# Kernel tuning notes

Hardware: AMD Instinct MI355X
Metric: run time of the kernel (lower is better)

Reference implementation:

```python
import jax, jax.numpy as jnp
import numpy as np

N = 50000   # nodes
E = 800000  # edges per edge type
H = 4       # attention heads
C = 64      # per-head out channels
EPS = 1e-5  # batchnorm eps


def gat_conv(x, ei, W, a_s, a_d, b):
    # PyG GATConv with add_self_loops=True, concat=True, negative_slope=0.2
    h = (x @ W).reshape(-1, H, C)                      # [N,H,C]
    sl = jnp.arange(N)
    src = jnp.concatenate([ei[0], sl])                 # [E+N]
    dst = jnp.concatenate([ei[1], sl])
    al_s = (h * a_s).sum(-1)                           # [N,H]
    al_d = (h * a_d).sum(-1)
    e = jax.nn.leaky_relu(al_s[src] + al_d[dst], 0.2)  # [E+N,H]
    m = jax.ops.segment_max(e, dst, num_segments=N)    # segment softmax over dst
    ex = jnp.exp(e - m[dst])
    s = jax.ops.segment_sum(ex, dst, num_segments=N)
    alpha = ex / (s[dst] + 1e-16)                      # [E+N,H]
    out = jax.ops.segment_sum(alpha[:, :, None] * h[src], dst, num_segments=N)
    return out.reshape(N, H * C) + b


def bn(x, g, b):
    mu = x.mean(0)
    v = jnp.var(x, 0)
    return g * (x - mu) * jax.lax.rsqrt(v + EPS) + b


def setup_inputs() -> dict:
    key = jax.random.key(0)
    ks = jax.random.split(key, 20)
    p = {}
    p["x"] = jax.random.normal(ks[0], (N, 128), jnp.float32)
    p["edge_index_spatial"] = jax.random.randint(ks[1], (2, E), 0, N)
    p["edge_index_temporal"] = jax.random.randint(ks[2], (2, E), 0, N)
    ins = [128, 256, 256, 256]
    k = 3
    for i in range(4):
        sc = 1.0 / np.sqrt(ins[i]).astype(np.float32)
        p[f"W{i+1}"] = jax.random.normal(ks[k], (ins[i], H * C), jnp.float32) * sc; k += 1
        p[f"as{i+1}"] = jax.random.normal(ks[k], (H, C), jnp.float32) * 0.1; k += 1
        p[f"ad{i+1}"] = jax.random.normal(ks[k], (H, C), jnp.float32) * 0.1; k += 1
        p[f"b{i+1}"] = jnp.zeros((H * C,), jnp.float32)
        p[f"g{i+1}"] = jnp.ones((H * C,), jnp.float32)
        p[f"be{i+1}"] = jnp.zeros((H * C,), jnp.float32)
    p["Wl"] = jax.random.normal(ks[k], (H * C, 32), jnp.float32) * (1.0 / 16.0)
    p["bl"] = jnp.zeros((32,), jnp.float32)
    return p


def reference(x, edge_index_spatial, edge_index_temporal,
              W1, as1, ad1, b1, g1, be1,
              W2, as2, ad2, b2, g2, be2,
              W3, as3, ad3, b3, g3, be3,
              W4, as4, ad4, b4, g4, be4,
              Wl, bl):
    h = jax.nn.relu(bn(gat_conv(x, edge_index_spatial, W1, as1, ad1, b1), g1, be1))
    h = jax.nn.relu(bn(gat_conv(h, edge_index_spatial, W2, as2, ad2, b2), g2, be2))
    h = jax.nn.relu(bn(gat_conv(h, edge_index_temporal, W3, as3, ad3, b3), g3, be3))
    h = jax.nn.relu(bn(gat_conv(h, edge_index_temporal, W4, as4, ad4, b4), g4, be4))
    return h @ Wl + bl
```

## Files before the change

kernel.cpp:

```cpp
#include <hip/hip_runtime.h>
#include <hip/hip_bf16.h>
#include <hip/hip_fp16.h>
#include <math.h>

#define N_NODES 50000
#define N_EDGES 800000
#define NH 4
#define HC 256
#define TOT_E (N_EDGES + N_NODES)
#define SCAN_NB ((N_NODES + 255) / 256)

typedef __attribute__((ext_vector_type(8))) short short8;
typedef __attribute__((ext_vector_type(4))) float f32x4;

static __device__ __forceinline__ float lrelu(float x) { return x >= 0.f ? x : 0.2f * x; }

static __device__ __forceinline__ unsigned short bf16_rne(float x) {
    unsigned int u = __float_as_uint(x);
    u += 0x7fff + ((u >> 16) & 1);
    return (unsigned short)(u >> 16);
}

__global__ __launch_bounds__(256) void count_kernel(const int* __restrict__ ei,
                                                    int* __restrict__ cnt) {
    int i = blockIdx.x * blockDim.x + threadIdx.x;
    if (i >= TOT_E) return;
    int dst = (i < N_EDGES) ? ei[N_EDGES + i] : (i - N_EDGES);
    atomicAdd(&cnt[dst], 1);
}

__global__ __launch_bounds__(256) void scan1_kernel(const int* __restrict__ cnt,
                                                    int* __restrict__ offs,
                                                    int* __restrict__ bsum) {
    __shared__ int sm[256];
    const int t = threadIdx.x;
    const int base = blockIdx.x * 256;
    int v = (base + t < N_NODES) ? cnt[base + t] : 0;
    sm[t] = v;
    __syncthreads();
#pragma unroll
    for (int d = 1; d < 256; d <<= 1) {
        int add = (t >= d) ? sm[t - d] : 0;
        __syncthreads();
        sm[t] += add;
        __syncthreads();
    }
    if (base + t < N_NODES) offs[base + t] = sm[t] - v;
    if (t == 255) bsum[blockIdx.x] = sm[255];
}

__global__ __launch_bounds__(256) void scan2_kernel(int* __restrict__ bsum,
                                                    int* __restrict__ total) {
    __shared__ int sm[256];
    const int t = threadIdx.x;
    int v = (t < SCAN_NB) ? bsum[t] : 0;
    sm[t] = v;
    __syncthreads();
#pragma unroll
    for (int d = 1; d < 256; d <<= 1) {
        int add = (t >= d) ? sm[t - d] : 0;
        __syncthreads();
        sm[t] += add;
        __syncthreads();
    }
    if (t < SCAN_NB) bsum[t] = sm[t] - v;
    if (t == 255) *total = sm[255];
}

__global__ __launch_bounds__(256) void scan3_kernel(int* __restrict__ offs,
                                                    const int* __restrict__ bsum) {
    int i = blockIdx.x * blockDim.x + threadIdx.x;
    if (i < N_NODES) offs[i] += bsum[i >> 8];
}

__global__ __launch_bounds__(256) void scatter_kernel(const int* __restrict__ ei,
                                                      const int* __restrict__ offs,
                                                      int* __restrict__ cursor,
                                                      int* __restrict__ ssrc) {
    int i = blockIdx.x * blockDim.x + threadIdx.x;
    if (i >= TOT_E) return;
    int src, dst;
    if (i < N_EDGES) { src = ei[i]; dst = ei[N_EDGES + i]; }
    else             { src = i - N_EDGES; dst = src; }
    int pos = offs[dst] + atomicAdd(&cursor[dst], 1);
    ssrc[pos] = src;
}

__global__ __launch_bounds__(256) void gemm_kernel(const float* __restrict__ A,
                                                   const float* __restrict__ B,
                                                   __half* __restrict__ C,
                                                   const float* __restrict__ bnscale,
                                                   const float* __restrict__ bnshift,
                                                   const float* __restrict__ a_s,
                                                   const float* __restrict__ a_d,
                                                   float* __restrict__ als,
                                                   float* __restrict__ ald,
                                                   int M, int K) {
    __shared__ unsigned short Ah[128][40], Al[128][40];
    __shared__ unsigned short Bh[128][40], Bl[128][40];
    const int t = threadIdx.x;
    const int l = t & 63;
    const int w = t >> 6;
    const int wr = w >> 1, wc = w & 1;
    const int fr = l & 15;
    const int kg = (l >> 4) << 3;
    const int bm = blockIdx.x * 128;
    const int bn = blockIdx.y * 128;
    const int ra = t >> 1, ka = (t & 1) << 4;
    const int nb = (t & 31) << 2, kb = (t >> 5) << 2;

    f32x4 acc[4][4] = {};

    for (int k0 = 0; k0 < K; k0 += 32) {
        {
            const int row = bm + ra;
#pragma unroll
            for (int i = 0; i < 4; ++i) {
                const int kk = ka + 4 * i;
                float4 a4 = make_float4(0.f, 0.f, 0.f, 0.f);
                if (row < M) a4 = *(const float4*)(A + (size_t)row * K + k0 + kk);
                if (bnscale) {
                    float4 sc = *(const float4*)(bnscale + k0 + kk);
                    float4 sh = *(const float4*)(bnshift + k0 + kk);
                    a4.x = fmaxf(0.f, fmaf(a4.x, sc.x, sh.x));
                    a4.y = fmaxf(0.f, fmaf(a4.y, sc.y, sh.y));
                    a4.z = fmaxf(0.f, fmaf(a4.z, sc.z, sh.z));
                    a4.w = fmaxf(0.f, fmaf(a4.w, sc.w, sh.w));
                }
                unsigned short h[4], lo[4];
                float v[4] = {a4.x, a4.y, a4.z, a4.w};
#pragma unroll
                for (int q = 0; q < 4; ++q) {
                    h[q] = bf16_rne(v[q]);
                    float hf = __uint_as_float((unsigned int)h[q] << 16);
                    lo[q] = bf16_rne(v[q] - hf);
                }
                *(uint2*)&Ah[ra][kk] = *(uint2*)h;
                *(uint2*)&Al[ra][kk] = *(uint2*)lo;
            }
        }
        {
            float4 bv[4];
#pragma unroll
            for (int i = 0; i < 4; ++i)
                bv[i] = *(const float4*)(B + (size_t)(k0 + kb + i) * HC + bn + nb);
#pragma unroll
            for (int c = 0; c < 4; ++c) {
                float v[4] = {c == 0 ? bv[0].x : c == 1 ? bv[0].y : c == 2 ? bv[0].z : bv[0].w,
                              c == 0 ? bv[1].x : c == 1 ? bv[1].y : c == 2 ? bv[1].z : bv[1].w,
                              c == 0 ? bv[2].x : c == 1 ? bv[2].y : c == 2 ? bv[2].z : bv[2].w,
                              c == 0 ? bv[3].x : c == 1 ? bv[3].y : c == 2 ? bv[3].z : bv[3].w};
                unsigned short h[4], lo[4];
#pragma unroll
                for (int q = 0; q < 4; ++q) {
                    h[q] = bf16_rne(v[q]);
                    float hf = __uint_as_float((unsigned int)h[q] << 16);
                    lo[q] = bf16_rne(v[q] - hf);
                }
                *(uint2*)&Bh[nb + c][kb] = *(uint2*)h;
                *(uint2*)&Bl[nb + c][kb] = *(uint2*)lo;
            }
        }
        __syncthreads();
        short8 ahf[4], alf[4], bhf[4], blf[4];
#pragma unroll
        for (int m = 0; m < 4; ++m) {
            ahf[m] = *(const short8*)&Ah[wr * 64 + m * 16 + fr][kg];
            alf[m] = *(const short8*)&Al[wr * 64 + m * 16 + fr][kg];
        }
#pragma unroll
        for (int n = 0; n < 4; ++n) {
            bhf[n] = *(const short8*)&Bh[wc * 64 + n * 16 + fr][kg];
            blf[n] = *(const short8*)&Bl[wc * 64 + n * 16 + fr][kg];
        }
#pragma unroll
        for (int m = 0; m < 4; ++m)
#pragma unroll
            for (int n = 0; n < 4; ++n) {
                acc[m][n] = __builtin_amdgcn_mfma_f32_16x16x32_bf16(ahf[m], bhf[n], acc[m][n], 0, 0, 0);
                acc[m][n] = __builtin_amdgcn_mfma_f32_16x16x32_bf16(ahf[m], blf[n], acc[m][n], 0, 0, 0);
                acc[m][n] = __builtin_amdgcn_mfma_f32_16x16x32_bf16(alf[m], bhf[n], acc[m][n], 0, 0, 0);
            }
        __syncthreads();
    }

#pragma unroll
    for (int m = 0; m < 4; ++m) {
        const int row0 = bm + wr * 64 + m * 16 + ((l >> 4) << 2);
#pragma unroll
        for (int n = 0; n < 4; ++n) {
            const int col = bn + wc * 64 + n * 16 + fr;
#pragma unroll
            for (int r = 0; r < 4; ++r) {
                if (row0 + r < M)
                    C[(size_t)(row0 + r) * HC + col] = __float2half(acc[m][n][r]);
            }
        }
    }
    const int hw = (bn >> 6) + wc;
    float asv[4], adv[4];
#pragma unroll
    for (int n = 0; n < 4; ++n) {
        const int col = bn + wc * 64 + n * 16 + fr;
        asv[n] = a_s[col];
        adv[n] = a_d[col];
    }
#pragma unroll
    for (int m = 0; m < 4; ++m) {
        const int row0 = bm + wr * 64 + m * 16 + ((l >> 4) << 2);
#pragma unroll
        for (int r = 0; r < 4; ++r) {
            float ps = 0.f, pd = 0.f;
#pragma unroll
            for (int n = 0; n < 4; ++n) {
                ps = fmaf(acc[m][n][r], asv[n], ps);
                pd = fmaf(acc[m][n][r], adv[n], pd);
            }
#pragma unroll
            for (int d = 1; d < 16; d <<= 1) {
                ps += __shfl_xor(ps, d, 64);
                pd += __shfl_xor(pd, d, 64);
            }
            if (fr == 0 && row0 + r < M) {
                als[(row0 + r) * NH + hw] = ps;
                ald[(row0 + r) * NH + hw] = pd;
            }
        }
    }
}

__global__ __launch_bounds__(256) void gat_edge_kernel(const __half* __restrict__ h,
                                                       const int* __restrict__ offs,
                                                       const int* __restrict__ ssrc,
                                                       const float* __restrict__ als,
                                                       const float* __restrict__ ald,
                                                       const float* __restrict__ bias,
                                                       float* __restrict__ out) {
    __shared__ float ex_sm[4][64][NH];
    __shared__ int   src_sm[4][64];
    const int lane = threadIdx.x & 63;
    const int w = threadIdx.x >> 6;
    const int v = (blockIdx.x << 2) + w;
    if (v >= N_NODES) return;
    const int hh = lane >> 4;
    const float4 aldv4 = *(const float4*)(ald + v * NH);
    const int beg = offs[v], end = offs[v + 1];

    float4 m4 = make_float4(-INFINITY, -INFINITY, -INFINITY, -INFINITY);
    float4 s4 = make_float4(0.f, 0.f, 0.f, 0.f);
    float ax = 0.f, ay = 0.f, az = 0.f, aw = 0.f;

    for (int c0 = beg; c0 < end; c0 += 64) {
        const int n = min(64, end - c0);
        const int s0 = ssrc[c0];
        int srcl = s0;
        float4 e4 = make_float4(-INFINITY, -INFINITY, -INFINITY, -INFINITY);
        if (lane < n) {
            srcl = ssrc[c0 + lane];
            float4 a4 = *(const float4*)(als + srcl * NH);
            e4.x = lrelu(a4.x + aldv4.x);
            e4.y = lrelu(a4.y + aldv4.y);
            e4.z = lrelu(a4.z + aldv4.z);
            e4.w = lrelu(a4.w + aldv4.w);
        }
        float4 cm = e4;
#pragma unroll
        for (int d = 1; d < 64; d <<= 1) {
            cm.x = fmaxf(cm.x, __shfl_xor(cm.x, d, 64));
            cm.y = fmaxf(cm.y, __shfl_xor(cm.y, d, 64));
            cm.z = fmaxf(cm.z, __shfl_xor(cm.z, d, 64));
            cm.w = fmaxf(cm.w, __shfl_xor(cm.w, d, 64));
        }
        const float4 mn = make_float4(fmaxf(m4.x, cm.x), fmaxf(m4.y, cm.y),
                                      fmaxf(m4.z, cm.z), fmaxf(m4.w, cm.w));
        const float4 r4 = make_float4(__expf(m4.x - mn.x), __expf(m4.y - mn.y),
                                      __expf(m4.z - mn.z), __expf(m4.w - mn.w));
        float4 ex4;
        ex4.x = __expf(e4.x - mn.x);
        ex4.y = __expf(e4.y - mn.y);
        ex4.z = __expf(e4.z - mn.z);
        ex4.w = __expf(e4.w - mn.w);
        src_sm[w][lane] = srcl;
        *(float4*)&ex_sm[w][lane][0] = ex4;
        float4 se = ex4;
#pragma unroll
        for (int d = 1; d < 64; d <<= 1) {
            se.x += __shfl_xor(se.x, d, 64);
            se.y += __shfl_xor(se.y, d, 64);
            se.z += __shfl_xor(se.z, d, 64);
            se.w += __shfl_xor(se.w, d, 64);
        }
        s4 = make_float4(fmaf(s4.x, r4.x, se.x), fmaf(s4.y, r4.y, se.y),
                         fmaf(s4.z, r4.z, se.z), fmaf(s4.w, r4.w, se.w));
        const float rh = hh == 0 ? r4.x : hh == 1 ? r4.y : hh == 2 ? r4.z : r4.w;
        ax *= rh; ay *= rh; az *= rh; aw *= rh;
        m4 = mn;

        const int trip = (n + 7) & ~7;
        int sj[8]; float wj[8];
#pragma unroll
        for (int q = 0; q < 8; ++q) { sj[q] = src_sm[w][q]; wj[q] = ex_sm[w][q][hh]; }
        const int co = lane << 2;
        for (int j = 0; j < trip; j += 8) {
            uint2 raw[8];
#pragma unroll
            for (int q = 0; q < 8; ++q)
                raw[q] = *(const uint2*)(h + (size_t)sj[q] * HC + co);
            float u[8];
#pragma unroll
            for (int q = 0; q < 8; ++q) u[q] = wj[q];
            if (j + 8 < trip) {
#pragma unroll
                for (int q = 0; q < 8; ++q) {
                    sj[q] = src_sm[w][j + 8 + q];
                    wj[q] = ex_sm[w][j + 8 + q][hh];
                }
            }
#pragma unroll
            for (int q = 0; q < 8; ++q) {
                const __half2 lo = *reinterpret_cast<const __half2*>(&raw[q].x);
                const __half2 hi = *reinterpret_cast<const __half2*>(&raw[q].y);
                const float2 f0 = __half22float2(lo);
                const float2 f1 = __half22float2(hi);
                ax = fmaf(u[q], f0.x, ax); ay = fmaf(u[q], f0.y, ay);
                az = fmaf(u[q], f1.x, az); aw = fmaf(u[q], f1.y, aw);
            }
        }
    }

    const float sh = hh == 0 ? s4.x : hh == 1 ? s4.y : hh == 2 ? s4.z : s4.w;
    const float inv = 1.f / (sh + 1e-16f);
    const float4 b4 = *(const float4*)(bias + (lane << 2));
    *(float4*)(out + (size_t)v * HC + (lane << 2)) =
        make_float4(fmaf(ax, inv, b4.x), fmaf(ay, inv, b4.y),
                    fmaf(az, inv, b4.z), fmaf(aw, inv, b4.w));
}

__global__ __launch_bounds__(256) void bn_stats_kernel(const float* __restrict__ y,
                                                       double* __restrict__ sum,
                                                       double* __restrict__ sqsum) {
    const int t = threadIdx.x;
    const int r0 = blockIdx.x * 128;
    const int r1 = min(r0 + 128, N_NODES);
    float s = 0.f, q = 0.f;
    for (int r = r0; r < r1; ++r) {
        float v = y[(size_t)r * HC + t];
        s += v;
        q = fmaf(v, v, q);
    }
    atomicAdd(&sum[t], (double)s);
    atomicAdd(&sqsum[t], (double)q);
}

__global__ void bn_finalize_kernel(const double* __restrict__ sum,
                                   const double* __restrict__ sqsum,
                                   const float* __restrict__ g,
                                   const float* __restrict__ be,
                                   float* __restrict__ scale,
                                   float* __restrict__ shift) {
    int t = threadIdx.x;
    double mean = sum[t] / (double)N_NODES;
    double var = sqsum[t] / (double)N_NODES - mean * mean;
    float sc = g[t] * rsqrtf((float)var + 1e-5f);
    scale[t] = sc;
    shift[t] = be[t] - (float)mean * sc;
}

__global__ __launch_bounds__(256) void linear_kernel(const float* __restrict__ y,
                                                     const float* __restrict__ Wl,
                                                     const float* __restrict__ bl,
                                                     const float* __restrict__ scale,
                                                     const float* __restrict__ shift,
                                                     float* __restrict__ out) {
    __shared__ float Wls[256 * 32];
    __shared__ float scs[256], shs[256];
    const int t = threadIdx.x;
    for (int i = t; i < 256 * 32; i += 256) Wls[i] = Wl[i];
    scs[t] = scale[t];
    shs[t] = shift[t];
    __syncthreads();
    int gid = blockIdx.x * 256 + t;
    if (gid >= N_NODES * 32) return;
    int n = gid >> 5, j = gid & 31;
    float acc = bl[j];
    const float4* yrow = (const float4*)(y + (size_t)n * HC);
#pragma unroll
    for (int k4 = 0; k4 < 64; ++k4) {
        float4 y4 = yrow[k4];
        int k = k4 << 2;
        y4.x = fmaxf(0.f, fmaf(y4.x, scs[k + 0], shs[k + 0]));
        y4.y = fmaxf(0.f, fmaf(y4.y, scs[k + 1], shs[k + 1]));
        y4.z = fmaxf(0.f, fmaf(y4.z, scs[k + 2], shs[k + 2]));
        y4.w = fmaxf(0.f, fmaf(y4.w, scs[k + 3], shs[k + 3]));
        acc = fmaf(y4.x, Wls[(k + 0) * 32 + j], acc);
        acc = fmaf(y4.y, Wls[(k + 1) * 32 + j], acc);
        acc = fmaf(y4.z, Wls[(k + 2) * 32 + j], acc);
        acc = fmaf(y4.w, Wls[(k + 3) * 32 + j], acc);
    }
    out[gid] = acc;
}

extern "C" void kernel_launch(void* const* d_in, const int* in_sizes, int n_in,
                              void* d_out, int out_size, void* d_ws, size_t ws_size,
                              hipStream_t stream) {
    const float* x     = (const float*)d_in[0];
    const int* ei_sp   = (const int*)d_in[1];
    const int* ei_tp   = (const int*)d_in[2];
    const float* Wl    = (const float*)d_in[27];
    const float* bl    = (const float*)d_in[28];

    char* ws = (char*)d_ws;
    size_t off = 0;
    auto alloc = [&](size_t bytes) -> char* {
        char* p = ws + off;
        off = (off + bytes + 255) & ~(size_t)255;
        return p;
    };
    __half* buf0   = (__half*)alloc((size_t)N_NODES * HC * 2);
    float* buf1    = (float*)alloc((size_t)N_NODES * HC * 4);
    float* als     = (float*)alloc((size_t)N_NODES * NH * 4);
    float* ald     = (float*)alloc((size_t)N_NODES * NH * 4);
    int*   offs_sp = (int*)alloc((size_t)(N_NODES + 1) * 4);
    int*   offs_tp = (int*)alloc((size_t)(N_NODES + 1) * 4);
    int*   src_sp  = (int*)alloc((size_t)TOT_E * 4);
    int*   src_tp  = (int*)alloc((size_t)TOT_E * 4);
    int*   cnt     = (int*)alloc((size_t)N_NODES * 4);
    int*   bsum    = (int*)alloc((size_t)SCAN_NB * 4);
    double* bnsum  = (double*)alloc(256 * 8 * 2);
    double* bnsq   = bnsum + 256;
    float* scale   = (float*)alloc(256 * 4);
    float* shift   = (float*)alloc(256 * 4);
    (void)ws_size; (void)in_sizes; (void)n_in; (void)out_size;

    const int EB = (TOT_E + 255) / 256;

    hipMemsetAsync(cnt, 0, (size_t)N_NODES * 4, stream);
    count_kernel<<<EB, 256, 0, stream>>>(ei_sp, cnt);
    scan1_kernel<<<SCAN_NB, 256, 0, stream>>>(cnt, offs_sp, bsum);
    scan2_kernel<<<1, 256, 0, stream>>>(bsum, offs_sp + N_NODES);
    scan3_kernel<<<SCAN_NB, 256, 0, stream>>>(offs_sp, bsum);
    hipMemsetAsync(cnt, 0, (size_t)N_NODES * 4, stream);
    scatter_kernel<<<EB, 256, 0, stream>>>(ei_sp, offs_sp, cnt, src_sp);

    hipMemsetAsync(cnt, 0, (size_t)N_NODES * 4, stream);
    count_kernel<<<EB, 256, 0, stream>>>(ei_tp, cnt);
    scan1_kernel<<<SCAN_NB, 256, 0, stream>>>(cnt, offs_tp, bsum);
    scan2_kernel<<<1, 256, 0, stream>>>(bsum, offs_tp + N_NODES);
    scan3_kernel<<<SCAN_NB, 256, 0, stream>>>(offs_tp, bsum);
    hipMemsetAsync(cnt, 0, (size_t)N_NODES * 4, stream);
    scatter_kernel<<<EB, 256, 0, stream>>>(ei_tp, offs_tp, cnt, src_tp);

    const int NB4 = (N_NODES + 3) / 4;
    const dim3 ggrid((N_NODES + 127) / 128, 2);
    for (int L = 0; L < 4; ++L) {
        const float* in = (L == 0) ? x : buf1;
        const int K = (L == 0) ? 128 : 256;
        const float* bns = (L == 0) ? nullptr : scale;
        const float* bnh = (L == 0) ? nullptr : shift;
        const int* offs = (L < 2) ? offs_sp : offs_tp;
        const int* ssrc = (L < 2) ? src_sp : src_tp;
        const int base = 3 + L * 6;
        const float* W  = (const float*)d_in[base + 0];
        const float* as_ = (const float*)d_in[base + 1];
        const float* ad_ = (const float*)d_in[base + 2];
        const float* b_  = (const float*)d_in[base + 3];
        const float* g_  = (const float*)d_in[base + 4];
        const float* be_ = (const float*)d_in[base + 5];

        gemm_kernel<<<ggrid, 256, 0, stream>>>(in, W, buf0, bns, bnh,
                                               as_, ad_, als, ald, N_NODES, K);
        gat_edge_kernel<<<NB4, 256, 0, stream>>>(buf0, offs, ssrc, als, ald, b_, buf1);

        hipMemsetAsync(bnsum, 0, 256 * 8 * 2, stream);
        bn_stats_kernel<<<(N_NODES + 127) / 128, 256, 0, stream>>>(buf1, bnsum, bnsq);
        bn_finalize_kernel<<<1, 256, 0, stream>>>(bnsum, bnsq, g_, be_, scale, shift);
    }

    linear_kernel<<<(N_NODES * 32 + 255) / 256, 256, 0, stream>>>(buf1, Wl, bl,
                                                                  scale, shift,
                                                                  (float*)d_out);
}
```

Measured before the change: 1.057 ms.

## Merge CSR builds, pre-split GEMM operands to bf16 hi/lo, widen edge gather

Builds both edge-type CSR structures in a single set of count/scan/scatter launches. Splits activations and weights into bf16 hi/lo arrays in separate kernels so the GEMM only does vector loads of bf16 data. The edge aggregation kernel now gathers 16-byte rows, with two edges processed per wave half. BN finalize is folded into the split and linear kernels. This removes launches and per-tile conversion work but adds an extra pass over activations and more workspace.

```diff
diff --git a/kernel.cpp b/kernel.cpp
--- a/kernel.cpp
+++ b/kernel.cpp
@@ -8,24 +8,32 @@
 #define NH 4
 #define HC 256
 #define TOT_E (N_EDGES + N_NODES)
-#define SCAN_NB ((N_NODES + 255) / 256)
+#define NT2 (2 * N_NODES)
+#define NB2 ((NT2 + 255) / 256)
 
 typedef __attribute__((ext_vector_type(8))) short short8;
 typedef __attribute__((ext_vector_type(4))) float f32x4;
+typedef unsigned short ushort_t;
 
 static __device__ __forceinline__ float lrelu(float x) { return x >= 0.f ? x : 0.2f * x; }
 
-static __device__ __forceinline__ unsigned short bf16_rne(float x) {
+static __device__ __forceinline__ ushort_t bf16_rne(float x) {
     unsigned int u = __float_as_uint(x);
     u += 0x7fff + ((u >> 16) & 1);
-    return (unsigned short)(u >> 16);
-}
-
-__global__ __launch_bounds__(256) void count_kernel(const int* __restrict__ ei,
-                                                    int* __restrict__ cnt) {
+    return (ushort_t)(u >> 16);
+}
+
+__global__ __launch_bounds__(256) void count2_kernel(const int* __restrict__ ei_sp,
+                                                     const int* __restrict__ ei_tp,
+                                                     int* __restrict__ cnt) {
     int i = blockIdx.x * blockDim.x + threadIdx.x;
-    if (i >= TOT_E) return;
-    int dst = (i < N_EDGES) ? ei[N_EDGES + i] : (i - N_EDGES);
+    if (i >= 2 * TOT_E) return;
+    int dst;
+    if (i < TOT_E) dst = (i < N_EDGES) ? ei_sp[N_EDGES + i] : (i - N_EDGES);
+    else {
+        int j = i - TOT_E;
+        dst = N_NODES + ((j < N_EDGES) ? ei_tp[N_EDGES + j] : (j - N_EDGES));
+    }
     atomicAdd(&cnt[dst], 1);
 }
 
@@ -35,7 +43,7 @@
     __shared__ int sm[256];
     const int t = threadIdx.x;
     const int base = blockIdx.x * 256;
-    int v = (base + t < N_NODES) ? cnt[base + t] : 0;
+    int v = (base + t < NT2) ? cnt[base + t] : 0;
     sm[t] = v;
     __syncthreads();
 #pragma unroll
@@ -45,59 +53,142 @@
         sm[t] += add;
         __syncthreads();
     }
-    if (base + t < N_NODES) offs[base + t] = sm[t] - v;
+    if (base + t < NT2) offs[base + t] = sm[t] - v;
     if (t == 255) bsum[blockIdx.x] = sm[255];
 }
 
-__global__ __launch_bounds__(256) void scan2_kernel(int* __restrict__ bsum,
+__global__ __launch_bounds__(512) void scan2_kernel(int* __restrict__ bsum,
                                                     int* __restrict__ total) {
-    __shared__ int sm[256];
+    __shared__ int sm[512];
     const int t = threadIdx.x;
-    int v = (t < SCAN_NB) ? bsum[t] : 0;
+    int v = (t < NB2) ? bsum[t] : 0;
     sm[t] = v;
     __syncthreads();
 #pragma unroll
-    for (int d = 1; d < 256; d <<= 1) {
+    for (int d = 1; d < 512; d <<= 1) {
         int add = (t >= d) ? sm[t - d] : 0;
         __syncthreads();
         sm[t] += add;
         __syncthreads();
     }
-    if (t < SCAN_NB) bsum[t] = sm[t] - v;
-    if (t == 255) *total = sm[255];
+    if (t < NB2) bsum[t] = sm[t] - v;
+    if (t == 511) *total = sm[511];
 }
 
 __global__ __launch_bounds__(256) void scan3_kernel(int* __restrict__ offs,
                                                     const int* __restrict__ bsum) {
     int i = blockIdx.x * blockDim.x + threadIdx.x;
-    if (i < N_NODES) offs[i] += bsum[i >> 8];
-}
-
-__global__ __launch_bounds__(256) void scatter_kernel(const int* __restrict__ ei,
-                                                      const int* __restrict__ offs,
-                                                      int* __restrict__ cursor,
-                                                      int* __restrict__ ssrc) {
+    if (i < NT2) offs[i] += bsum[i >> 8];
+}
+
+__global__ __launch_bounds__(256) void scatter2_kernel(const int* __restrict__ ei_sp,
+                                                       const int* __restrict__ ei_tp,
+                                                       const int* __restrict__ offs,
+                                                       int* __restrict__ cursor,
+                                                       int* __restrict__ ssrc) {
     int i = blockIdx.x * blockDim.x + threadIdx.x;
-    if (i >= TOT_E) return;
-    int src, dst;
-    if (i < N_EDGES) { src = ei[i]; dst = ei[N_EDGES + i]; }
-    else             { src = i - N_EDGES; dst = src; }
-    int pos = offs[dst] + atomicAdd(&cursor[dst], 1);
+    if (i >= 2 * TOT_E) return;
+    int src, dstIdx;
+    if (i < TOT_E) {
+        src = (i < N_EDGES) ? ei_sp[i] : (i - N_EDGES);
+        dstIdx = (i < N_EDGES) ? ei_sp[N_EDGES + i] : (i - N_EDGES);
+    } else {
+        int j = i - TOT_E;
+        src = (j < N_EDGES) ? ei_tp[j] : (j - N_EDGES);
+        dstIdx = N_NODES + ((j < N_EDGES) ? ei_tp[N_EDGES + j] : (j - N_EDGES));
+    }
+    int pos = offs[dstIdx] + atomicAdd(&cursor[dstIdx], 1);
     ssrc[pos] = src;
 }
 
-__global__ __launch_bounds__(256) void gemm_kernel(const float* __restrict__ A,
-                                                   const float* __restrict__ B,
+__global__ __launch_bounds__(256) void split_x_kernel(const float* __restrict__ x,
+                                                      ushort_t* __restrict__ Ah,
+                                                      ushort_t* __restrict__ Al) {
+    int i = blockIdx.x * 256 + threadIdx.x;
+    float4 v = ((const float4*)x)[i];
+    float a[4] = {v.x, v.y, v.z, v.w};
+    ushort_t h[4], lo[4];
+#pragma unroll
+    for (int q = 0; q < 4; ++q) {
+        h[q] = bf16_rne(a[q]);
+        float hf = __uint_as_float((unsigned int)h[q] << 16);
+        lo[q] = bf16_rne(a[q] - hf);
+    }
+    *(uint2*)(Ah + (size_t)i * 4) = *(uint2*)h;
+    *(uint2*)(Al + (size_t)i * 4) = *(uint2*)lo;
+}
+
+__global__ __launch_bounds__(256) void split_h_kernel(const float* __restrict__ y,
+                                                      const double* __restrict__ sum,
+                                                      const double* __restrict__ sqsum,
+                                                      const float* __restrict__ g,
+                                                      const float* __restrict__ be,
+                                                      ushort_t* __restrict__ Ah,
+                                                      ushort_t* __restrict__ Al) {
+    __shared__ float scs[256], shs[256];
+    const int t = threadIdx.x;
+    {
+        double mean = sum[t] / (double)N_NODES;
+        double var = sqsum[t] / (double)N_NODES - mean * mean;
+        float sc = g[t] * rsqrtf((float)var + 1e-5f);
+        scs[t] = sc;
+        shs[t] = be[t] - (float)mean * sc;
+    }
+    __syncthreads();
+    int i = blockIdx.x * 256 + t;
+    int c4 = (i & 63) << 2;
+    float4 v = ((const float4*)y)[i];
+    float a[4] = {fmaxf(0.f, fmaf(v.x, scs[c4 + 0], shs[c4 + 0])),
+                  fmaxf(0.f, fmaf(v.y, scs[c4 + 1], shs[c4 + 1])),
+                  fmaxf(0.f, fmaf(v.z, scs[c4 + 2], shs[c4 + 2])),
+                  fmaxf(0.f, fmaf(v.w, scs[c4 + 3], shs[c4 + 3]))};
+    ushort_t h[4], lo[4];
+#pragma unroll
+    for (int q = 0; q < 4; ++q) {
+        h[q] = bf16_rne(a[q]);
+        float hf = __uint_as_float((unsigned int)h[q] << 16);
+        lo[q] = bf16_rne(a[q] - hf);
+    }
+    *(uint2*)(Ah + (size_t)i * 4) = *(uint2*)h;
+    *(uint2*)(Al + (size_t)i * 4) = *(uint2*)lo;
+}
+
+__global__ __launch_bounds__(256) void split_ball_kernel(const float* __restrict__ W1,
+                                                         const float* __restrict__ W2,
+                                                         const float* __restrict__ W3,
+                                                         const float* __restrict__ W4,
+                                                         ushort_t* __restrict__ Bh,
+                                                         ushort_t* __restrict__ Bl) {
+    int i = blockIdx.x * 256 + threadIdx.x;
+    int loc, kshift;
+    const float* W;
+    if (i < 32768) { W = W1; loc = i; kshift = 7; }
+    else {
+        int L = (i - 32768) >> 16;
+        W = L == 0 ? W2 : L == 1 ? W3 : W4;
+        loc = (i - 32768) & 65535;
+        kshift = 8;
+    }
+    int c = loc >> kshift, kl = loc & ((1 << kshift) - 1);
+    float v = W[(size_t)kl * 256 + c];
+    ushort_t h = bf16_rne(v);
+    float hf = __uint_as_float((unsigned int)h << 16);
+    Bh[i] = h;
+    Bl[i] = bf16_rne(v - hf);
+}
+
+__global__ __launch_bounds__(256) void gemm_kernel(const ushort_t* __restrict__ Ahg,
+                                                   const ushort_t* __restrict__ Alg,
+                                                   const ushort_t* __restrict__ Bhg,
+                                                   const ushort_t* __restrict__ Blg,
                                                    __half* __restrict__ C,
-                                                   const float* __restrict__ bnscale,
-                                                   const float* __restrict__ bnshift,
                                                    const float* __restrict__ a_s,
                                                    const float* __restrict__ a_d,
                                                    float* __restrict__ als,
                                                    float* __restrict__ ald,
                                                    int M, int K) {
-    __shared__ unsigned short Ah[128][40], Al[128][40];
-    __shared__ unsigned short Bh[128][40], Bl[128][40];
+    __shared__ ushort_t Ah[128][40], Al[128][40];
+    __shared__ ushort_t Bh[128][40], Bl[128][40];
     const int t = threadIdx.x;
     const int l = t & 63;
     const int w = t >> 6;
@@ -106,62 +197,31 @@
     const int kg = (l >> 4) << 3;
     const int bm = blockIdx.x * 128;
     const int bn = blockIdx.y * 128;
-    const int ra = t >> 1, ka = (t & 1) << 4;
-    const int nb = (t & 31) << 2, kb = (t >> 5) << 2;
+    const int sr = t >> 1;
+    const int sk = (t & 1) << 4;
 
     f32x4 acc[4][4] = {};
 
     for (int k0 = 0; k0 < K; k0 += 32) {
-        {
-            const int row = bm + ra;
-#pragma unroll
-            for (int i = 0; i < 4; ++i) {
-                const int kk = ka + 4 * i;
-                float4 a4 = make_float4(0.f, 0.f, 0.f, 0.f);
-                if (row < M) a4 = *(const float4*)(A + (size_t)row * K + k0 + kk);
-                if (bnscale) {
-                    float4 sc = *(const float4*)(bnscale + k0 + kk);
-                    float4 sh = *(const float4*)(bnshift + k0 + kk);
-                    a4.x = fmaxf(0.f, fmaf(a4.x, sc.x, sh.x));
-                    a4.y = fmaxf(0.f, fmaf(a4.y, sc.y, sh.y));
-                    a4.z = fmaxf(0.f, fmaf(a4.z, sc.z, sh.z));
-                    a4.w = fmaxf(0.f, fmaf(a4.w, sc.w, sh.w));
-                }
-                unsigned short h[4], lo[4];
-                float v[4] = {a4.x, a4.y, a4.z, a4.w};
-#pragma unroll
-                for (int q = 0; q < 4; ++q) {
-                    h[q] = bf16_rne(v[q]);
-                    float hf = __uint_as_float((unsigned int)h[q] << 16);
-                    lo[q] = bf16_rne(v[q] - hf);
-                }
-                *(uint2*)&Ah[ra][kk] = *(uint2*)h;
-                *(uint2*)&Al[ra][kk] = *(uint2*)lo;
-            }
-        }
-        {
-            float4 bv[4];
-#pragma unroll
-            for (int i = 0; i < 4; ++i)
-                bv[i] = *(const float4*)(B + (size_t)(k0 + kb + i) * HC + bn + nb);
-#pragma unroll
-            for (int c = 0; c < 4; ++c) {
-                float v[4] = {c == 0 ? bv[0].x : c == 1 ? bv[0].y : c == 2 ? bv[0].z : bv[0].w,
-                              c == 0 ? bv[1].x : c == 1 ? bv[1].y : c == 2 ? bv[1].z : bv[1].w,
-                              c == 0 ? bv[2].x : c == 1 ? bv[2].y : c == 2 ? bv[2].z : bv[2].w,
-                              c == 0 ? bv[3].x : c == 1 ? bv[3].y : c == 2 ? bv[3].z : bv[3].w};
-                unsigned short h[4], lo[4];
-#pragma unroll
-                for (int q = 0; q < 4; ++q) {
-                    h[q] = bf16_rne(v[q]);
-                    float hf = __uint_as_float((unsigned int)h[q] << 16);
-                    lo[q] = bf16_rne(v[q] - hf);
-                }
-                *(uint2*)&Bh[nb + c][kb] = *(uint2*)h;
-                *(uint2*)&Bl[nb + c][kb] = *(uint2*)lo;
-            }
-        }
+        const size_t abase = (size_t)(bm + sr) * K + k0 + sk;
+        uint4 a0 = {}, a1 = {}, l0 = {}, l1 = {};
+        if (bm + sr < M) {
+            a0 = *(const uint4*)(Ahg + abase);
+            a1 = *(const uint4*)(Ahg + abase + 8);
+            l0 = *(const uint4*)(Alg + abase);
+            l1 = *(const uint4*)(Alg + abase + 8);
+        }
+        const size_t bbase = (size_t)(bn + sr) * K + k0 + sk;
+        uint4 b0 = *(const uint4*)(Bhg + bbase);
+        uint4 b1 = *(const uint4*)(Bhg + bbase + 8);
+        uint4 c0 = *(const uint4*)(Blg + bbase);
+        uint4 c1 = *(const uint4*)(Blg + bbase + 8);
+        *(uint4*)&Ah[sr][sk] = a0; *(uint4*)&Ah[sr][sk + 8] = a1;
+        *(uint4*)&Al[sr][sk] = l0; *(uint4*)&Al[sr][sk + 8] = l1;
+        *(uint4*)&Bh[sr][sk] = b0; *(uint4*)&Bh[sr][sk + 8] = b1;
+        *(uint4*)&Bl[sr][sk] = c0; *(uint4*)&Bl[sr][sk + 8] = c1;
         __syncthreads();
+
         short8 ahf[4], alf[4], bhf[4], blf[4];
 #pragma unroll
         for (int m = 0; m < 4; ++m) {
@@ -241,19 +301,19 @@
     const int lane = threadIdx.x & 63;
     const int w = threadIdx.x >> 6;
     const int v = (blockIdx.x << 2) + w;
-    if (v >= N_NODES) return;
-    const int hh = lane >> 4;
+    const int ehalf = lane >> 5;
+    const int cl = lane & 31;
+    const int hh2 = cl >> 3;
     const float4 aldv4 = *(const float4*)(ald + v * NH);
     const int beg = offs[v], end = offs[v + 1];
 
     float4 m4 = make_float4(-INFINITY, -INFINITY, -INFINITY, -INFINITY);
     float4 s4 = make_float4(0.f, 0.f, 0.f, 0.f);
-    float ax = 0.f, ay = 0.f, az = 0.f, aw = 0.f;
+    float acc8[8] = {0.f};
 
     for (int c0 = beg; c0 < end; c0 += 64) {
         const int n = min(64, end - c0);
-        const int s0 = ssrc[c0];
-        int srcl = s0;
+        int srcl = ssrc[c0];
         float4 e4 = make_float4(-INFINITY, -INFINITY, -INFINITY, -INFINITY);
         if (lane < n) {
             srcl = ssrc[c0 + lane];
@@ -282,58 +342,60 @@
         ex4.w = __expf(e4.w - mn.w);
         src_sm[w][lane] = srcl;
         *(float4*)&ex_sm[w][lane][0] = ex4;
-        float4 se = ex4;
-#pragma unroll
-        for (int d = 1; d < 64; d <<= 1) {
-            se.x += __shfl_xor(se.x, d, 64);
-            se.y += __shfl_xor(se.y, d, 64);
-            se.z += __shfl_xor(se.z, d, 64);
-            se.w += __shfl_xor(se.w, d, 64);
-        }
-        s4 = make_float4(fmaf(s4.x, r4.x, se.x), fmaf(s4.y, r4.y, se.y),
-                         fmaf(s4.z, r4.z, se.z), fmaf(s4.w, r4.w, se.w));
-        const float rh = hh == 0 ? r4.x : hh == 1 ? r4.y : hh == 2 ? r4.z : r4.w;
-        ax *= rh; ay *= rh; az *= rh; aw *= rh;
+        s4 = make_float4(fmaf(s4.x, r4.x, ex4.x), fmaf(s4.y, r4.y, ex4.y),
+                         fmaf(s4.z, r4.z, ex4.z), fmaf(s4.w, r4.w, ex4.w));
+        const float rh2 = hh2 == 0 ? r4.x : hh2 == 1 ? r4.y : hh2 == 2 ? r4.z : r4.w;
+#pragma unroll
+        for (int i = 0; i < 8; ++i) acc8[i] *= rh2;
         m4 = mn;
 
         const int trip = (n + 7) & ~7;
-        int sj[8]; float wj[8];
-#pragma unroll
-        for (int q = 0; q < 8; ++q) { sj[q] = src_sm[w][q]; wj[q] = ex_sm[w][q][hh]; }
-        const int co = lane << 2;
+        const int co2 = cl << 3;
         for (int j = 0; j < trip; j += 8) {
-            uint2 raw[8];
-#pragma unroll
-            for (int q = 0; q < 8; ++q)
-                raw[q] = *(const uint2*)(h + (size_t)sj[q] * HC + co);
-            float u[8];
-#pragma unroll
-            for (int q = 0; q < 8; ++q) u[q] = wj[q];
-            if (j + 8 < trip) {
-#pragma unroll
-                for (int q = 0; q < 8; ++q) {
-                    sj[q] = src_sm[w][j + 8 + q];
-                    wj[q] = ex_sm[w][j + 8 + q][hh];
+            uint4 raw[4];
+            float u[4];
+#pragma unroll
+            for (int q = 0; q < 4; ++q) {
+                const int e = j + 2 * q + ehalf;
+                const int s = src_sm[w][e];
+                raw[q] = *(const uint4*)(h + (size_t)s * HC + co2);
+                u[q] = ex_sm[w][e][hh2];
+            }
+#pragma unroll
+            for (int q = 0; q < 4; ++q) {
+                const __half2* p = reinterpret_cast<const __half2*>(&raw[q]);
+#pragma unroll
+                for (int z = 0; z < 4; ++z) {
+                    const float2 f = __half22float2(p[z]);
+                    acc8[2 * z]     = fmaf(u[q], f.x, acc8[2 * z]);
+                    acc8[2 * z + 1] = fmaf(u[q], f.y, acc8[2 * z + 1]);
                 }
             }
-#pragma unroll
-            for (int q = 0; q < 8; ++q) {
-                const __half2 lo = *reinterpret_cast<const __half2*>(&raw[q].x);
-                const __half2 hi = *reinterpret_cast<const __half2*>(&raw[q].y);
-                const float2 f0 = __half22float2(lo);
-                const float2 f1 = __half22float2(hi);
-                ax = fmaf(u[q], f0.x, ax); ay = fmaf(u[q], f0.y, ay);
-                az = fmaf(u[q], f1.x, az); aw = fmaf(u[q], f1.y, aw);
-            }
-        }
-    }
-
-    const float sh = hh == 0 ? s4.x : hh == 1 ? s4.y : hh == 2 ? s4.z : s4.w;
+        }
+    }
+
+#pragma unroll
+    for (int i = 0; i < 8; ++i) acc8[i] += __shfl_xor(acc8[i], 32, 64);
+#pragma unroll
+    for (int d = 1; d < 64; d <<= 1) {
+        s4.x += __shfl_xor(s4.x, d, 64);
+        s4.y += __shfl_xor(s4.y, d, 64);
+        s4.z += __shfl_xor(s4.z, d, 64);
+        s4.w += __shfl_xor(s4.w, d, 64);
+    }
+    const float sh = hh2 == 0 ? s4.x : hh2 == 1 ? s4.y : hh2 == 2 ? s4.z : s4.w;
     const float inv = 1.f / (sh + 1e-16f);
-    const float4 b4 = *(const float4*)(bias + (lane << 2));
-    *(float4*)(out + (size_t)v * HC + (lane << 2)) =
-        make_float4(fmaf(ax, inv, b4.x), fmaf(ay, inv, b4.y),
-                    fmaf(az, inv, b4.z), fmaf(aw, inv, b4.w));
+    if (ehalf == 0) {
+        const int cb = cl << 3;
+        const float4 b0 = *(const float4*)(bias + cb);
+        const float4 b1 = *(const float4*)(bias + cb + 4);
+        *(float4*)(out + (size_t)v * HC + cb) =
+            make_float4(fmaf(acc8[0], inv, b0.x), fmaf(acc8[1], inv, b0.y),
+                        fmaf(acc8[2], inv, b0.z), fmaf(acc8[3], inv, b0.w));
+        *(float4*)(out + (size_t)v * HC + cb + 4) =
+            make_float4(fmaf(acc8[4], inv, b1.x), fmaf(acc8[5], inv, b1.y),
+                        fmaf(acc8[6], inv, b1.z), fmaf(acc8[7], inv, b1.w));
+    }
 }
 
 __global__ __launch_bounds__(256) void bn_stats_kernel(const float* __restrict__ y,
@@ -352,35 +414,27 @@
     atomicAdd(&sqsum[t], (double)q);
 }
 
-__global__ void bn_finalize_kernel(const double* __restrict__ sum,
-                                   const double* __restrict__ sqsum,
-                                   const float* __restrict__ g,
-                                   const float* __restrict__ be,
-                                   float* __restrict__ scale,
-                                   float* __restrict__ shift) {
-    int t = threadIdx.x;
-    double mean = sum[t] / (double)N_NODES;
-    double var = sqsum[t] / (double)N_NODES - mean * mean;
-    float sc = g[t] * rsqrtf((float)var + 1e-5f);
-    scale[t] = sc;
-    shift[t] = be[t] - (float)mean * sc;
-}
-
 __global__ __launch_bounds__(256) void linear_kernel(const float* __restrict__ y,
                                                      const float* __restrict__ Wl,
                                                      const float* __restrict__ bl,
-                                                     const float* __restrict__ scale,
-                                                     const float* __restrict__ shift,
+                                                     const double* __restrict__ sum,
+                                                     const double* __restrict__ sqsum,
+                                                     const float* __restrict__ g,
+                                                     const float* __restrict__ be,
                                                      float* __restrict__ out) {
     __shared__ float Wls[256 * 32];
     __shared__ float scs[256], shs[256];
     const int t = threadIdx.x;
+    {
+        double mean = sum[t] / (double)N_NODES;
+        double var = sqsum[t] / (double)N_NODES - mean * mean;
+        float sc = g[t] * rsqrtf((float)var + 1e-5f);
+        scs[t] = sc;
+        shs[t] = be[t] - (float)mean * sc;
+    }
     for (int i = t; i < 256 * 32; i += 256) Wls[i] = Wl[i];
-    scs[t] = scale[t];
-    shs[t] = shift[t];
     __syncthreads();
     int gid = blockIdx.x * 256 + t;
-    if (gid >= N_NODES * 32) return;
     int n = gid >> 5, j = gid & 31;
     float acc = bl[j];
     const float4* yrow = (const float4*)(y + (size_t)n * HC);
@@ -403,11 +457,11 @@
 extern "C" void kernel_launch(void* const* d_in, const int* in_sizes, int n_in,
                               void* d_out, int out_size, void* d_ws, size_t ws_size,
                               hipStream_t stream) {
-    const float* x     = (const float*)d_in[0];
-    const int* ei_sp   = (const int*)d_in[1];
-    const int* ei_tp   = (const int*)d_in[2];
-    const float* Wl    = (const float*)d_in[27];
-    const float* bl    = (const float*)d_in[28];
+    const float* x   = (const float*)d_in[0];
+    const int* ei_sp = (const int*)d_in[1];
+    const int* ei_tp = (const int*)d_in[2];
+    const float* Wl  = (const float*)d_in[27];
+    const float* bl  = (const float*)d_in[28];
 
     char* ws = (char*)d_ws;
     size_t off = 0;
@@ -416,67 +470,63 @@
         off = (off + bytes + 255) & ~(size_t)255;
         return p;
     };
+    ushort_t* AhA  = (ushort_t*)alloc((size_t)N_NODES * HC * 2);
+    ushort_t* AlA  = (ushort_t*)alloc((size_t)N_NODES * HC * 2);
     __half* buf0   = (__half*)alloc((size_t)N_NODES * HC * 2);
     float* buf1    = (float*)alloc((size_t)N_NODES * HC * 4);
     float* als     = (float*)alloc((size_t)N_NODES * NH * 4);
     float* ald     = (float*)alloc((size_t)N_NODES * NH * 4);
-    int*   offs_sp = (int*)alloc((size_t)(N_NODES + 1) * 4);
-    int*   offs_tp = (int*)alloc((size_t)(N_NODES + 1) * 4);
-    int*   src_sp  = (int*)alloc((size_t)TOT_E * 4);
-    int*   src_tp  = (int*)alloc((size_t)TOT_E * 4);
-    int*   cnt     = (int*)alloc((size_t)N_NODES * 4);
-    int*   bsum    = (int*)alloc((size_t)SCAN_NB * 4);
+    int*  offs_all = (int*)alloc((size_t)(NT2 + 1) * 4);
+    int*  ssrc_all = (int*)alloc((size_t)2 * TOT_E * 4);
+    int*  cnt_all  = (int*)alloc((size_t)2 * NT2 * 4);
+    int*  cursor   = cnt_all + NT2;
+    int*  bsum     = (int*)alloc((size_t)NB2 * 4);
+    ushort_t* BhA  = (ushort_t*)alloc((size_t)229376 * 2);
+    ushort_t* BlA  = (ushort_t*)alloc((size_t)229376 * 2);
     double* bnsum  = (double*)alloc(256 * 8 * 2);
     double* bnsq   = bnsum + 256;
-    float* scale   = (float*)alloc(256 * 4);
-    float* shift   = (float*)alloc(256 * 4);
     (void)ws_size; (void)in_sizes; (void)n_in; (void)out_size;
 
-    const int EB = (TOT_E + 255) / 256;
-
-    hipMemsetAsync(cnt, 0, (size_t)N_NODES * 4, stream);
-    count_kernel<<<EB, 256, 0, stream>>>(ei_sp, cnt);
-    scan1_kernel<<<SCAN_NB, 256, 0, stream>>>(cnt, offs_sp, bsum);
-    scan2_kernel<<<1, 256, 0, stream>>>(bsum, offs_sp + N_NODES);
-    scan3_kernel<<<SCAN_NB, 256, 0, stream>>>(offs_sp, bsum);
-    hipMemsetAsync(cnt, 0, (size_t)N_NODES * 4, stream);
-    scatter_kernel<<<EB, 256, 0, stream>>>(ei_sp, offs_sp, cnt, src_sp);
-
-    hipMemsetAsync(cnt, 0, (size_t)N_NODES * 4, stream);
-    count_kernel<<<EB, 256, 0, stream>>>(ei_tp, cnt);
-    scan1_kernel<<<SCAN_NB, 256, 0, stream>>>(cnt, offs_tp, bsum);
-    scan2_kernel<<<1, 256, 0, stream>>>(bsum, offs_tp + N_NODES);
-    scan3_kernel<<<SCAN_NB, 256, 0, stream>>>(offs_tp, bsum);
-    hipMemsetAsync(cnt, 0, (size_t)N_NODES * 4, stream);
-    scatter_kernel<<<EB, 256, 0, stream>>>(ei_tp, offs_tp, cnt, src_tp);
-
-    const int NB4 = (N_NODES + 3) / 4;
+    const int EB2 = (2 * TOT_E + 255) / 256;
+    const int offB[4] = {0, 32768, 98304, 163840};
+
+    hipMemsetAsync(cnt_all, 0, (size_t)2 * NT2 * 4, stream);
+    count2_kernel<<<EB2, 256, 0, stream>>>(ei_sp, ei_tp, cnt_all);
+    scan1_kernel<<<NB2, 256, 0, stream>>>(cnt_all, offs_all, bsum);
+    scan2_kernel<<<1, 512, 0, stream>>>(bsum, offs_all + NT2);
+    scan3_kernel<<<NB2, 256, 0, stream>>>(offs_all, bsum);
+    scatter2_kernel<<<EB2, 256, 0, stream>>>(ei_sp, ei_tp, offs_all, cursor, ssrc_all);
+
+    split_x_kernel<<<N_NODES * 32 / 256, 256, 0, stream>>>(x, AhA, AlA);
+    split_ball_kernel<<<896, 256, 0, stream>>>((const float*)d_in[3], (const float*)d_in[9],
+                                               (const float*)d_in[15], (const float*)d_in[21],
+                                               BhA, BlA);
+
+    const int NB4 = N_NODES / 4;
     const dim3 ggrid((N_NODES + 127) / 128, 2);
     for (int L = 0; L < 4; ++L) {
-        const float* in = (L == 0) ? x : buf1;
         const int K = (L == 0) ? 128 : 256;
-        const float* bns = (L == 0) ? nullptr : scale;
-        const float* bnh = (L == 0) ? nullptr : shift;
-        const int* offs = (L < 2) ? offs_sp : offs_tp;
-        const int* ssrc = (L < 2) ? src_sp : src_tp;
+        const int* offs = (L < 2) ? offs_all : (offs_all + N_NODES);
         const int base = 3 + L * 6;
-        const float* W  = (const float*)d_in[base + 0];
         const float* as_ = (const float*)d_in[base + 1];
         const float* ad_ = (const float*)d_in[base + 2];
         const float* b_  = (const float*)d_in[base + 3];
-        const float* g_  = (const float*)d_in[base + 4];
-        const float* be_ = (const float*)d_in[base + 5];
-
-        gemm_kernel<<<ggrid, 256, 0, stream>>>(in, W, buf0, bns, bnh,
-                                               as_, ad_, als, ald, N_NODES, K);
-        gat_edge_kernel<<<NB4, 256, 0, stream>>>(buf0, offs, ssrc, als, ald, b_, buf1);
+
+        if (L > 0) {
+            const int pbase = 3 + (L - 1) * 6;
+            split_h_kernel<<<N_NODES * 64 / 256, 256, 0, stream>>>(
+                buf1, bnsum, bnsq, (const float*)d_in[pbase + 4],
+                (const float*)d_in[pbase + 5], AhA, AlA);
+        }
+        gemm_kernel<<<ggrid, 256, 0, stream>>>(AhA, AlA, BhA + offB[L], BlA + offB[L],
+                                               buf0, as_, ad_, als, ald, N_NODES, K);
+        gat_edge_kernel<<<NB4, 256, 0, stream>>>(buf0, offs, ssrc_all, als, ald, b_, buf1);
 
         hipMemsetAsync(bnsum, 0, 256 * 8 * 2, stream);
         bn_stats_kernel<<<(N_NODES + 127) / 128, 256, 0, stream>>>(buf1, bnsum, bnsq);
-        bn_finalize_kernel<<<1, 256, 0, stream>>>(bnsum, bnsq, g_, be_, scale, shift);
-    }
-
-    linear_kernel<<<(N_NODES * 32 + 255) / 256, 256, 0, stream>>>(buf1, Wl, bl,
-                                                                  scale, shift,
-                                                                  (float*)d_out);
-}
+    }
+
+    linear_kernel<<<N_NODES * 32 / 256, 256, 0, stream>>>(
+        buf1, Wl, bl, bnsum, bnsq, (const float*)d_in[25], (const float*)d_in[26],
+        (float*)d_out);
+}
```

Result: faster. 1.021 ms (-3.4%).
